# Kernel optimization log

Hardware: AMD Instinct MI355X
Metric: run time of the kernel (lower is better)

Reference implementation:

```python
import jax, jax.numpy as jnp
import numpy as np

EPS = 0.01  # Normalizer eps
N_NODES = 100000
N_EDGES = 1600000


def gcn_conv(x, edge_index, W, b, n_nodes):
    """PyG-style GCNConv: x @ W, symmetric-normalized aggregation with self-loops, + bias."""
    src = jnp.concatenate([edge_index[0], jnp.arange(n_nodes)])  # [E+N]
    dst = jnp.concatenate([edge_index[1], jnp.arange(n_nodes)])  # [E+N]
    h = x @ W  # [N, out]
    ones = jnp.ones_like(dst, dtype=h.dtype)
    deg = jax.ops.segment_sum(ones, dst, num_segments=n_nodes)  # [N]
    dinv = jnp.where(deg > 0, jax.lax.rsqrt(deg), 0.0)
    norm = dinv[src] * dinv[dst]  # [E+N]
    msgs = h[src] * norm[:, None]  # [E+N, out]  (largest intermediate)
    out = jax.ops.segment_sum(msgs, dst, num_segments=n_nodes)  # [N, out]
    return out + b


def setup_inputs() -> dict:
    key = jax.random.key(0)
    k = jax.random.split(key, 6)
    x = jax.random.normal(k[0], (N_NODES, 16), dtype=jnp.float32)
    edge_index = jax.random.randint(k[1], (2, N_EDGES), 0, N_NODES)
    W1 = jax.random.normal(k[2], (16, 64), dtype=jnp.float32) * 0.25
    b1 = jax.random.normal(k[3], (64,), dtype=jnp.float32) * 0.1
    W3 = jax.random.normal(k[4], (64, 32), dtype=jnp.float32) * 0.125
    b3 = jax.random.normal(k[5], (32,), dtype=jnp.float32) * 0.1
    return {"x": x, "edge_index": edge_index, "W1": W1, "b1": b1, "W3": W3, "b3": b3}


def reference(x, edge_index, W1, b1, W3, b3):
    n = x.shape[0]
    h = jax.nn.relu(gcn_conv(x, edge_index, W1, b1, n))
    h = jax.nn.relu(gcn_conv(h, edge_index, W3, b3, n))
    # Normalizer: sequential Welford observe over all nodes then normalize with
    # FINAL stats == population mean / clamped population variance.
    mean = h.mean(axis=0)  # [32]
    var = jnp.maximum(((h - mean) ** 2).mean(axis=0), EPS)  # [32]
    return (h - mean) * jax.lax.rsqrt(var)
```

## Files before the change

### kernel.cpp

```cpp
#include <hip/hip_runtime.h>
#include <hip/hip_fp16.h>

#define EPS 0.01f
#define SCAN_BS 512
#define NCHUNKS 256
#define BUCKET_SHIFT 9
#define BUCKET_SZ (1 << BUCKET_SHIFT)
#define STAGE_CAP 16384


__global__ __launch_bounds__(SCAN_BS) void k_scan_block(const int* __restrict__ in,
                                                        int* __restrict__ out,
                                                        int* __restrict__ bsum, int n) {
    __shared__ int sd[SCAN_BS];
    int t = threadIdx.x;
    int gid = blockIdx.x * SCAN_BS + t;
    int v = (gid < n) ? in[gid] : 0;
    sd[t] = v;
    __syncthreads();
    for (int off = 1; off < SCAN_BS; off <<= 1) {
        int x = (t >= off) ? sd[t - off] : 0;
        __syncthreads();
        sd[t] += x;
        __syncthreads();
    }
    if (gid < n) out[gid] = sd[t] - v;
    if (t == SCAN_BS - 1) bsum[blockIdx.x] = sd[t];
}

__global__ __launch_bounds__(SCAN_BS) void k_scan_tops(int* __restrict__ bsum, int nb) {
    __shared__ int sd[SCAN_BS];
    int t = threadIdx.x;
    int v = (t < nb) ? bsum[t] : 0;
    sd[t] = v;
    __syncthreads();
    for (int off = 1; off < SCAN_BS; off <<= 1) {
        int x = (t >= off) ? sd[t - off] : 0;
        __syncthreads();
        sd[t] += x;
        __syncthreads();
    }
    if (t < nb) bsum[t] = sd[t] - v;
}

__global__ __launch_bounds__(SCAN_BS) void k_scan_add(int* __restrict__ out,
                                                      const int* __restrict__ bsum, int n) {
    int gid = blockIdx.x * SCAN_BS + threadIdx.x;
    if (gid < n) out[gid] += bsum[blockIdx.x];
}


__global__ __launch_bounds__(256) void kA_bucket_hist(const int* __restrict__ dst,
                                                      int* __restrict__ bh, int e,
                                                      int nbuck, int ce) {
    extern __shared__ int hist[];
    int b = blockIdx.x, t = threadIdx.x;
    for (int i = t; i < nbuck; i += 256) hist[i] = 0;
    __syncthreads();
    int lo = b * ce, hi = min(lo + ce, e);
    for (int i = lo + t; i < hi; i += 256) atomicAdd(&hist[dst[i] >> BUCKET_SHIFT], 1);
    __syncthreads();
    for (int i = t; i < nbuck; i += 256) bh[i * NCHUNKS + b] = hist[i];
}

__global__ __launch_bounds__(256) void kC_bucket_scatter(const int* __restrict__ src,
                                                         const int* __restrict__ dst,
                                                         const int* __restrict__ bhs,
                                                         unsigned int* __restrict__ eb, int e,
                                                         int nbuck, int ce) {
    extern __shared__ int cur[];
    int b = blockIdx.x, t = threadIdx.x;
    for (int i = t; i < nbuck; i += 256) cur[i] = bhs[i * NCHUNKS + b];
    __syncthreads();
    int lo = b * ce, hi = min(lo + ce, e);
    for (int i = lo + t; i < hi; i += 256) {
        int s = src[i], d = dst[i];
        int pos = atomicAdd(&cur[d >> BUCKET_SHIFT], 1);
        eb[pos] = ((unsigned int)(d & (BUCKET_SZ - 1)) << 23) | (unsigned int)s;
    }
}

__global__ __launch_bounds__(256) void kDeg_fill_prescale(const unsigned int* __restrict__ eb,
                                                          const int* __restrict__ bhs,
                                                          const float* __restrict__ x,
                                                          int* __restrict__ degi,
                                                          float* __restrict__ dinv,
                                                          int* __restrict__ rowstart,
                                                          int* __restrict__ csr_src,
                                                          __half* __restrict__ xs,
                                                          float* __restrict__ partial,
                                                          int n, int nbuck, int e) {
    __shared__ unsigned int ebs[STAGE_CAP];
    __shared__ int hist[BUCKET_SZ];
    __shared__ int ps[256];
    __shared__ float dv[BUCKET_SZ];
    int k = blockIdx.x, t = threadIdx.x;
    if (k == 0 && t < 64) partial[t] = 0.f;
    for (int i = t; i < BUCKET_SZ; i += 256) hist[i] = 0;
    __syncthreads();
    int lo = bhs[k * NCHUNKS];
    int hi = (k + 1 < nbuck) ? bhs[(k + 1) * NCHUNKS] : e;
    int cnt = hi - lo;
    bool fits = (cnt <= STAGE_CAP);
    for (int i = t; i < cnt; i += 256) {
        unsigned int p = eb[lo + i];
        if (fits) ebs[i] = p;
        atomicAdd(&hist[p >> 23], 1);
    }
    __syncthreads();
    int a0 = hist[2 * t], a1 = hist[2 * t + 1];
    ps[t] = a0 + a1;
    __syncthreads();
    for (int off = 1; off < 256; off <<= 1) {
        int v = (t >= off) ? ps[t - off] : 0;
        __syncthreads();
        ps[t] += v;
        __syncthreads();
    }
    int excl = ps[t] - (a0 + a1);
    int node0 = k << BUCKET_SHIFT;
    int rs0 = lo + excl, rs1 = lo + excl + a0;
    {
        int nd0 = node0 + 2 * t, nd1 = nd0 + 1;
        float d0 = rsqrtf((float)a0 + 1.0f);
        float d1 = rsqrtf((float)a1 + 1.0f);
        dv[2 * t] = d0;
        dv[2 * t + 1] = d1;
        if (nd0 < n) {
            degi[nd0] = a0;
            dinv[nd0] = d0;
            rowstart[nd0] = rs0;
        }
        if (nd1 < n) {
            degi[nd1] = a1;
            dinv[nd1] = d1;
            rowstart[nd1] = rs1;
        }
    }
    __syncthreads();
    hist[2 * t] = rs0;
    hist[2 * t + 1] = rs1;
    for (int i = t; i < BUCKET_SZ * 16; i += 256) {
        int rl = i >> 4;
        int node = node0 + rl;
        if (node < n)
            xs[(size_t)node * 16 + (i & 15)] = __float2half(x[(size_t)node * 16 + (i & 15)] * dv[rl]);
    }
    __syncthreads();
    for (int i = t; i < cnt; i += 256) {
        unsigned int p = fits ? ebs[i] : eb[lo + i];
        int dl = (int)(p >> 23);
        int s = (int)(p & 0x7fffffu);
        int pos = atomicAdd(&hist[dl], 1);
        csr_src[pos] = s;
    }
}


__global__ __launch_bounds__(256) void k_l1_fused(const int* __restrict__ rowstart,
                                                  const int* __restrict__ degi,
                                                  const int* __restrict__ csr_src,
                                                  const float* __restrict__ dinv,
                                                  const __half* __restrict__ xs,
                                                  const float* __restrict__ W1,
                                                  const float* __restrict__ b1,
                                                  const float* __restrict__ W3,
                                                  __half* __restrict__ h2sA,
                                                  __half* __restrict__ h2sB, int n) {
    __shared__ float w1[16 * 64];
    __shared__ float w3[64 * 32];
    __shared__ float bs[64];
    __shared__ __align__(16) float a[16 * 16];
    __shared__ float z[16 * 64];
    int t = threadIdx.x;
    for (int i = t; i < 16 * 64; i += 256) w1[i] = W1[i];
    for (int i = t; i < 64 * 32; i += 256) w3[i] = W3[i];
    if (t < 64) bs[t] = b1[t];

    int row0 = blockIdx.x * 16;
    int wv = t >> 6;
    int lane = t & 63;
    int c2 = lane & 7;
    int slot = lane >> 3;
    const __half2* xs2 = (const __half2*)xs;

    for (int nid = 0; nid < 4; ++nid) {
        int node = row0 + wv * 4 + nid;
        if (node < n) {
            const int* sp = csr_src + rowstart[node];
            int deg = degi[node];
            int L = (deg + 7) >> 3;
            int base = slot * L;
            int end = min(base + L, deg);
            float ax = 0.f, ay = 0.f, bx = 0.f, by = 0.f;
            int k = base;
            for (; k + 2 <= end; k += 2) {
                int s0 = sp[k], s1 = sp[k + 1];
                float2 v0 = __half22float2(xs2[(size_t)s0 * 8 + c2]);
                float2 v1 = __half22float2(xs2[(size_t)s1 * 8 + c2]);
                ax += v0.x; ay += v0.y;
                bx += v1.x; by += v1.y;
            }
            if (k < end) {
                int s0 = sp[k];
                float2 v0 = __half22float2(xs2[(size_t)s0 * 8 + c2]);
                ax += v0.x; ay += v0.y;
            }
            float sx = ax + bx, sy = ay + by;
            sx += __shfl_xor(sx, 8);  sy += __shfl_xor(sy, 8);
            sx += __shfl_xor(sx, 16); sy += __shfl_xor(sy, 16);
            sx += __shfl_xor(sx, 32); sy += __shfl_xor(sy, 32);
            if (slot == 0) {
                float2 self = __half22float2(xs2[(size_t)node * 8 + c2]);
                float dn = dinv[node];
                int r = wv * 4 + nid;
                ((float2*)(a + r * 16))[c2] = make_float2(dn * (sx + self.x), dn * (sy + self.y));
            }
        }
    }
    __syncthreads();

    for (int i = t; i < 1024; i += 256) {
        int r = i >> 6, c = i & 63;
        float acc = bs[c];
#pragma unroll
        for (int k = 0; k < 16; ++k) acc += a[r * 16 + k] * w1[k * 64 + c];
        z[i] = acc > 0.f ? acc : 0.f;
    }
    __syncthreads();
    for (int i = t; i < 512; i += 256) {
        int r = i >> 5, c = i & 31;
        float acc = 0.f;
#pragma unroll
        for (int k = 0; k < 64; ++k) acc += z[r * 64 + k] * w3[k * 32 + c];
        int row = row0 + r;
        if (row < n) {
            __half hv = __float2half(acc * dinv[row]);
            if (c < 16) h2sA[(size_t)row * 16 + c] = hv;
            else        h2sB[(size_t)row * 16 + (c - 16)] = hv;
        }
    }
}


__global__ __launch_bounds__(256) void k_gather16x2_stats(const int* __restrict__ rowstart,
                                                          const int* __restrict__ degi,
                                                          const int* __restrict__ csr_src,
                                                          const float* __restrict__ dinv,
                                                          const __half* __restrict__ h2sA,
                                                          const __half* __restrict__ h2sB,
                                                          const float* __restrict__ b3,
                                                          float* __restrict__ out,
                                                          float* __restrict__ partial, int n) {
    int g = blockIdx.x;
    int half = (g >> 2) & 1;
    int nblk = (g >> 3) * 4 + (g & 3);
    int M = (n + 31) >> 5;
    if (nblk >= M) return;
    const __half2* h2 = (const __half2*)(half ? h2sB : h2sA);
    int col0 = half << 4;
    int t = threadIdx.x;
    int lane = t & 63;
    int c2 = lane & 7;
    int slot = lane >> 3;
    float2 bias = make_float2(b3[col0 + 2 * c2], b3[col0 + 2 * c2 + 1]);
    float s_x = 0.f, s_y = 0.f, q_x = 0.f, q_y = 0.f;
    for (int it = 0; it < 8; ++it) {
        int node = nblk * 32 + it * 4 + (t >> 6);
        if (node < n) {
            const int* sp = csr_src + rowstart[node];
            int deg = degi[node];
            int L = (deg + 7) >> 3;
            int base = slot * L;
            int end = min(base + L, deg);
            float ax = 0.f, ay = 0.f, bx = 0.f, by = 0.f;
            int k = base;
            for (; k + 2 <= end; k += 2) {
                int s0 = sp[k], s1 = sp[k + 1];
                float2 v0 = __half22float2(h2[(size_t)s0 * 8 + c2]);
                float2 v1 = __half22float2(h2[(size_t)s1 * 8 + c2]);
                ax += v0.x; ay += v0.y;
                bx += v1.x; by += v1.y;
            }
            if (k < end) {
                int s0 = sp[k];
                float2 v0 = __half22float2(h2[(size_t)s0 * 8 + c2]);
                ax += v0.x; ay += v0.y;
            }
            float sx = ax + bx, sy = ay + by;
            sx += __shfl_xor(sx, 8);  sy += __shfl_xor(sy, 8);
            sx += __shfl_xor(sx, 16); sy += __shfl_xor(sy, 16);
            sx += __shfl_xor(sx, 32); sy += __shfl_xor(sy, 32);
            if (slot == 0) {
                float2 self = __half22float2(h2[(size_t)node * 8 + c2]);
                float dn = dinv[node];
                float vx = dn * (sx + self.x) + bias.x;
                float vy = dn * (sy + self.y) + bias.y;
                vx = vx > 0.f ? vx : 0.f;
                vy = vy > 0.f ? vy : 0.f;
                ((float2*)(out + (size_t)node * 32 + col0))[c2] = make_float2(vx, vy);
                s_x += vx; s_y += vy;
                q_x += vx * vx; q_y += vy * vy;
            }
        }
    }
    __shared__ float ls[64], lq[64];
    int wv = t >> 6;
    if (lane < 8) {
        ls[wv * 16 + 2 * c2] = s_x;
        ls[wv * 16 + 2 * c2 + 1] = s_y;
        lq[wv * 16 + 2 * c2] = q_x;
        lq[wv * 16 + 2 * c2 + 1] = q_y;
    }
    __syncthreads();
    if (t < 16) {
        float a = 0.f, b = 0.f;
#pragma unroll
        for (int w = 0; w < 4; ++w) {
            a += ls[w * 16 + t];
            b += lq[w * 16 + t];
        }
        atomicAdd(&partial[col0 + t], a);
        atomicAdd(&partial[32 + col0 + t], b);
    }
}


__global__ void k_finalize(const float* __restrict__ partial, float* __restrict__ meaninv, int n) {
    int t = threadIdx.x;
    if (t < 32) {
        float invn = 1.0f / (float)n;
        float mean = partial[t] * invn;
        float var = partial[32 + t] * invn - mean * mean;
        var = var > EPS ? var : EPS;
        meaninv[t] = mean;
        meaninv[32 + t] = rsqrtf(var);
    }
}

__global__ void k_norm(float* __restrict__ h, const float* __restrict__ meaninv, int n) {
    long long idx = (long long)blockIdx.x * blockDim.x + threadIdx.x;
    if (idx < (long long)n * 32) {
        int c = (int)(idx & 31);
        h[idx] = (h[idx] - meaninv[c]) * meaninv[32 + c];
    }
}

extern "C" void kernel_launch(void* const* d_in, const int* in_sizes, int n_in,
                              void* d_out, int out_size, void* d_ws, size_t ws_size,
                              hipStream_t stream) {
    const float* x  = (const float*)d_in[0];
    const int* ei   = (const int*)d_in[1];
    const float* W1 = (const float*)d_in[2];
    const float* b1 = (const float*)d_in[3];
    const float* W3 = (const float*)d_in[4];
    const float* b3 = (const float*)d_in[5];

    const int N = in_sizes[0] / 16;
    const int E = in_sizes[1] / 2;
    const int* src = ei;
    const int* dst = ei + E;

    const int NBUCK = (N + BUCKET_SZ - 1) >> BUCKET_SHIFT;
    const int CE = (E + NCHUNKS - 1) / NCHUNKS;
    const int BH_TOTAL = NBUCK * NCHUNKS;

    char* ws = (char*)d_ws;
    int*   degi     = (int*)ws;          ws += (size_t)N * 4;
    float* dinv     = (float*)ws;        ws += (size_t)N * 4;
    int*   rowstart = (int*)ws;          ws += (size_t)N * 4;
    int*   bsum2    = (int*)ws;          ws += (size_t)SCAN_BS * 4;
    int*   bh       = (int*)ws;          ws += (size_t)BH_TOTAL * 4;
    int*   bhs      = (int*)ws;          ws += (size_t)BH_TOTAL * 4;
    unsigned int* eb = (unsigned int*)ws; ws += (size_t)E * 4;
    int*   csr_src  = (int*)ws;          ws += (size_t)E * 4;
    __half* xs      = (__half*)ws;       ws += (size_t)N * 16 * 2;
    __half* h2sA    = (__half*)ws;       ws += (size_t)N * 16 * 2;
    __half* h2sB    = (__half*)ws;       ws += (size_t)N * 16 * 2;
    float* partial  = (float*)ws;        ws += 64 * 4;
    float* meaninv  = (float*)ws;

    float* out = (float*)d_out;

    const int NB2 = (BH_TOTAL + SCAN_BS - 1) / SCAN_BS;

    kA_bucket_hist<<<NCHUNKS, 256, NBUCK * 4, stream>>>(dst, bh, E, NBUCK, CE);
    k_scan_block<<<NB2, SCAN_BS, 0, stream>>>(bh, bhs, bsum2, BH_TOTAL);
    k_scan_tops<<<1, SCAN_BS, 0, stream>>>(bsum2, NB2);
    k_scan_add<<<NB2, SCAN_BS, 0, stream>>>(bhs, bsum2, BH_TOTAL);
    kC_bucket_scatter<<<NCHUNKS, 256, NBUCK * 4, stream>>>(src, dst, bhs, eb, E, NBUCK, CE);

    kDeg_fill_prescale<<<NBUCK, 256, 0, stream>>>(eb, bhs, x, degi, dinv, rowstart,
                                                  csr_src, xs, partial, N, NBUCK, E);

    k_l1_fused<<<(N + 15) / 16, 256, 0, stream>>>(rowstart, degi, csr_src, dinv, xs,
                                                  W1, b1, W3, h2sA, h2sB, N);

    const int M = (N + 31) >> 5;
    const int G = ((M + 3) / 4) * 8;
    k_gather16x2_stats<<<G, 256, 0, stream>>>(rowstart, degi, csr_src, dinv, h2sA, h2sB,
                                              b3, out, partial, N);

    k_finalize<<<1, 64, 0, stream>>>(partial, meaninv, N);
    k_norm<<<((long long)N * 32 + 255) / 256, 256, 0, stream>>>(out, meaninv, N);
}
```

Before: 192.4 us.

## Aggregate layer-2 edges per dst bucket with LDS atomics instead of CSR gather

Replaces the per-node CSR gather for layer 2 with a per-bucket pass over the bucketed edge list. Each block accumulates source features into a 512-node shared-memory accumulator using LDS atomics, then applies self-loop, bias, ReLU and the statistics. This removes the per-node rowstart/degree indirection and the load imbalance across degrees, and the edge list is read in a coalesced stream. In exchange it adds shared-memory atomic contention, a 35KB LDS footprint that reduces occupancy, and fewer, larger blocks (one per 512-node bucket per half).

```diff
diff --git a/kernel.cpp b/kernel.cpp
--- a/kernel.cpp
+++ b/kernel.cpp
@@ -243,85 +243,90 @@
 }
 
 
-__global__ __launch_bounds__(256) void k_gather16x2_stats(const int* __restrict__ rowstart,
-                                                          const int* __restrict__ degi,
-                                                          const int* __restrict__ csr_src,
-                                                          const float* __restrict__ dinv,
-                                                          const __half* __restrict__ h2sA,
-                                                          const __half* __restrict__ h2sB,
-                                                          const float* __restrict__ b3,
-                                                          float* __restrict__ out,
-                                                          float* __restrict__ partial, int n) {
+__global__ __launch_bounds__(256) void k_l2_edge_stats(const unsigned int* __restrict__ eb,
+                                                       const int* __restrict__ bhs,
+                                                       const __half* __restrict__ h2sA,
+                                                       const __half* __restrict__ h2sB,
+                                                       const float* __restrict__ dinv,
+                                                       const float* __restrict__ b3,
+                                                       float* __restrict__ out,
+                                                       float* __restrict__ partial,
+                                                       int n, int nbuck, int e) {
+    __shared__ float acc[BUCKET_SZ][17];
+    __shared__ float redS[16], redQ[16];
     int g = blockIdx.x;
     int half = (g >> 2) & 1;
-    int nblk = (g >> 3) * 4 + (g & 3);
-    int M = (n + 31) >> 5;
-    if (nblk >= M) return;
+    int k = (g >> 3) * 4 + (g & 3);
+    if (k >= nbuck) return;
     const __half2* h2 = (const __half2*)(half ? h2sB : h2sA);
     int col0 = half << 4;
     int t = threadIdx.x;
+    for (int i = t; i < BUCKET_SZ * 17; i += 256) ((float*)acc)[i] = 0.f;
+    if (t < 16) { redS[t] = 0.f; redQ[t] = 0.f; }
+    __syncthreads();
+
+    int lo = bhs[k * NCHUNKS];
+    int hi = (k + 1 < nbuck) ? bhs[(k + 1) * NCHUNKS] : e;
+    int cnt = hi - lo;
     int lane = t & 63;
+    int wv = t >> 6;
     int c2 = lane & 7;
     int slot = lane >> 3;
-    float2 bias = make_float2(b3[col0 + 2 * c2], b3[col0 + 2 * c2 + 1]);
+
+    int i = wv * 8 + slot;
+    for (; i + 96 < cnt; i += 128) {
+        unsigned int p0 = eb[lo + i];
+        unsigned int p1 = eb[lo + i + 32];
+        unsigned int p2 = eb[lo + i + 64];
+        unsigned int p3 = eb[lo + i + 96];
+        float2 v0 = __half22float2(h2[(size_t)(p0 & 0x7fffffu) * 8 + c2]);
+        float2 v1 = __half22float2(h2[(size_t)(p1 & 0x7fffffu) * 8 + c2]);
+        float2 v2 = __half22float2(h2[(size_t)(p2 & 0x7fffffu) * 8 + c2]);
+        float2 v3 = __half22float2(h2[(size_t)(p3 & 0x7fffffu) * 8 + c2]);
+        int d0 = p0 >> 23, d1 = p1 >> 23, d2 = p2 >> 23, d3 = p3 >> 23;
+        atomicAdd(&acc[d0][2 * c2], v0.x);
+        atomicAdd(&acc[d0][2 * c2 + 1], v0.y);
+        atomicAdd(&acc[d1][2 * c2], v1.x);
+        atomicAdd(&acc[d1][2 * c2 + 1], v1.y);
+        atomicAdd(&acc[d2][2 * c2], v2.x);
+        atomicAdd(&acc[d2][2 * c2 + 1], v2.y);
+        atomicAdd(&acc[d3][2 * c2], v3.x);
+        atomicAdd(&acc[d3][2 * c2 + 1], v3.y);
+    }
+    for (; i < cnt; i += 32) {
+        unsigned int p = eb[lo + i];
+        float2 v = __half22float2(h2[(size_t)(p & 0x7fffffu) * 8 + c2]);
+        int d = p >> 23;
+        atomicAdd(&acc[d][2 * c2], v.x);
+        atomicAdd(&acc[d][2 * c2 + 1], v.y);
+    }
+    __syncthreads();
+
+    int node0 = k << BUCKET_SHIFT;
+    int c2p = t & 7;
+    float2 bias = make_float2(b3[col0 + 2 * c2p], b3[col0 + 2 * c2p + 1]);
     float s_x = 0.f, s_y = 0.f, q_x = 0.f, q_y = 0.f;
-    for (int it = 0; it < 8; ++it) {
-        int node = nblk * 32 + it * 4 + (t >> 6);
-        if (node < n) {
-            const int* sp = csr_src + rowstart[node];
-            int deg = degi[node];
-            int L = (deg + 7) >> 3;
-            int base = slot * L;
-            int end = min(base + L, deg);
-            float ax = 0.f, ay = 0.f, bx = 0.f, by = 0.f;
-            int k = base;
-            for (; k + 2 <= end; k += 2) {
-                int s0 = sp[k], s1 = sp[k + 1];
-                float2 v0 = __half22float2(h2[(size_t)s0 * 8 + c2]);
-                float2 v1 = __half22float2(h2[(size_t)s1 * 8 + c2]);
-                ax += v0.x; ay += v0.y;
-                bx += v1.x; by += v1.y;
-            }
-            if (k < end) {
-                int s0 = sp[k];
-                float2 v0 = __half22float2(h2[(size_t)s0 * 8 + c2]);
-                ax += v0.x; ay += v0.y;
-            }
-            float sx = ax + bx, sy = ay + by;
-            sx += __shfl_xor(sx, 8);  sy += __shfl_xor(sy, 8);
-            sx += __shfl_xor(sx, 16); sy += __shfl_xor(sy, 16);
-            sx += __shfl_xor(sx, 32); sy += __shfl_xor(sy, 32);
-            if (slot == 0) {
-                float2 self = __half22float2(h2[(size_t)node * 8 + c2]);
-                float dn = dinv[node];
-                float vx = dn * (sx + self.x) + bias.x;
-                float vy = dn * (sy + self.y) + bias.y;
-                vx = vx > 0.f ? vx : 0.f;
-                vy = vy > 0.f ? vy : 0.f;
-                ((float2*)(out + (size_t)node * 32 + col0))[c2] = make_float2(vx, vy);
-                s_x += vx; s_y += vy;
-                q_x += vx * vx; q_y += vy * vy;
-            }
-        }
-    }
-    __shared__ float ls[64], lq[64];
-    int wv = t >> 6;
-    if (lane < 8) {
-        ls[wv * 16 + 2 * c2] = s_x;
-        ls[wv * 16 + 2 * c2 + 1] = s_y;
-        lq[wv * 16 + 2 * c2] = q_x;
-        lq[wv * 16 + 2 * c2 + 1] = q_y;
-    }
+    for (int d = t >> 3; d < BUCKET_SZ; d += 32) {
+        int node = node0 + d;
+        if (node >= n) break;
+        float dn = dinv[node];
+        float2 self = __half22float2(h2[(size_t)node * 8 + c2p]);
+        float vx = dn * (acc[d][2 * c2p] + self.x) + bias.x;
+        float vy = dn * (acc[d][2 * c2p + 1] + self.y) + bias.y;
+        vx = vx > 0.f ? vx : 0.f;
+        vy = vy > 0.f ? vy : 0.f;
+        ((float2*)(out + (size_t)node * 32 + col0))[c2p] = make_float2(vx, vy);
+        s_x += vx; s_y += vy;
+        q_x += vx * vx; q_y += vy * vy;
+    }
+    atomicAdd(&redS[2 * c2p], s_x);
+    atomicAdd(&redS[2 * c2p + 1], s_y);
+    atomicAdd(&redQ[2 * c2p], q_x);
+    atomicAdd(&redQ[2 * c2p + 1], q_y);
     __syncthreads();
     if (t < 16) {
-        float a = 0.f, b = 0.f;
-#pragma unroll
-        for (int w = 0; w < 4; ++w) {
-            a += ls[w * 16 + t];
-            b += lq[w * 16 + t];
-        }
-        atomicAdd(&partial[col0 + t], a);
-        atomicAdd(&partial[32 + col0 + t], b);
+        atomicAdd(&partial[col0 + t], redS[t]);
+        atomicAdd(&partial[32 + col0 + t], redQ[t]);
     }
 }
 
@@ -396,10 +401,9 @@
     k_l1_fused<<<(N + 15) / 16, 256, 0, stream>>>(rowstart, degi, csr_src, dinv, xs,
                                                   W1, b1, W3, h2sA, h2sB, N);
 
-    const int M = (N + 31) >> 5;
-    const int G = ((M + 3) / 4) * 8;
-    k_gather16x2_stats<<<G, 256, 0, stream>>>(rowstart, degi, csr_src, dinv, h2sA, h2sB,
-                                              b3, out, partial, N);
+    const int G2 = ((NBUCK + 3) / 4) * 8;
+    k_l2_edge_stats<<<G2, 256, 0, stream>>>(eb, bhs, h2sA, h2sB, dinv, b3, out, partial,
+                                            N, NBUCK, E);
 
     k_finalize<<<1, 64, 0, stream>>>(partial, meaninv, N);
     k_norm<<<((long long)N * 32 + 255) / 256, 256, 0, stream>>>(out, meaninv, N);
```

Result: slower. 468.3 us (+143.4%).
